# Kernel optimization log

Hardware: AMD Instinct MI355X
Metric: run time of the kernel (lower is better)

## Reference

```python
import jax, jax.numpy as jnp
import numpy as np

B, T, D, E, K = 4, 2048, 1024, 8, 2

def setup_inputs() -> dict:
    key = jax.random.key(0)
    ks = jax.random.split(key, 4)
    scale = 1.0 / np.sqrt(D)
    return {
        "input_feat": jax.random.normal(ks[0], (B, T, D), dtype=jnp.float32),
        "delta": jax.random.normal(ks[1], (B, T, D), dtype=jnp.float32),
        "gate_W": jax.random.normal(ks[2], (E, D), dtype=jnp.float32) * scale,
        "gate_b": jnp.zeros((E,), dtype=jnp.float32),
        "expert_W": jax.random.normal(ks[3], (E, D, D), dtype=jnp.float32) * scale,
        "expert_b": jnp.zeros((E, D), dtype=jnp.float32),
    }

def reference(input_feat, delta, gate_W, gate_b, expert_W, expert_b):
    # Gating: logits [B,T,E], top-k over experts, softmax over the k logits
    gate_logits = jnp.einsum("btd,ed->bte", input_feat, gate_W) + gate_b
    topk_vals, topk_idx = jax.lax.top_k(gate_logits, K)          # [B,T,K]
    topk_weights = jax.nn.softmax(topk_vals, axis=-1)            # [B,T,K]

    # Dense per-expert linear on delta: [B,T,D,E] (torch Linear: x @ W.T + b)
    expert_outputs = jnp.einsum("btd,efd->btfe", delta, expert_W) + expert_b.T

    # Gather top-k expert outputs and weighted-combine
    idx = jnp.broadcast_to(topk_idx[:, :, None, :], (B, T, D, K))
    topk_outputs = jnp.take_along_axis(expert_outputs, idx, axis=-1)  # [B,T,D,K]
    weighted_output = jnp.sum(topk_outputs * topk_weights[:, :, None, :], axis=-1)
    return weighted_output
```

## Files before the change

### kernel.cpp

```cpp
#include <hip/hip_runtime.h>
#include <stdint.h>

#define NTOK 8192
#define D 1024
#define E 8
#define BM 128
#define BN 128
#define BK 64

typedef __attribute__((ext_vector_type(8))) short short8;
typedef __attribute__((ext_vector_type(4))) float f32x4;

__device__ __forceinline__ ushort f2bf(float f) {
  uint32_t x = __float_as_uint(f);
  x += 0x7FFFu + ((x >> 16) & 1u);
  return (ushort)(x >> 16);
}

#define NW4 2097152
#define ND4 2097152
#define NO4 2097152
__global__ __launch_bounds__(256) void convert_zero_kernel(
    const float* __restrict__ expert_W, const float* __restrict__ delta,
    ushort* __restrict__ Wb, ushort* __restrict__ Db,
    float* __restrict__ out, int* __restrict__ cnt) {
  int i = blockIdx.x * 256 + threadIdx.x;
  if (i < E) cnt[i] = 0;
  if (i < NW4) {
    float4 v = ((const float4*)expert_W)[i];
    ushort4 u; u.x = f2bf(v.x); u.y = f2bf(v.y); u.z = f2bf(v.z); u.w = f2bf(v.w);
    ((ushort4*)Wb)[i] = u;
  } else if (i < NW4 + ND4) {
    int j = i - NW4;
    float4 v = ((const float4*)delta)[j];
    ushort4 u; u.x = f2bf(v.x); u.y = f2bf(v.y); u.z = f2bf(v.z); u.w = f2bf(v.w);
    ((ushort4*)Db)[j] = u;
  } else {
    int j = i - NW4 - ND4;
    ((float4*)out)[j] = (float4){0.f, 0.f, 0.f, 0.f};
  }
}

__global__ __launch_bounds__(256) void gate_topk_kernel(
    const float* __restrict__ x, const float* __restrict__ gW,
    const float* __restrict__ gb,
    int* __restrict__ idx01, float2* __restrict__ w01) {
  int wave = threadIdx.x >> 6;
  int lane = threadIdx.x & 63;
  int t = blockIdx.x * 4 + wave;

  const float4* xr = (const float4*)(x + (size_t)t * D) + lane * 4;
  float acc[E];
#pragma unroll
  for (int e = 0; e < E; ++e) acc[e] = 0.f;
#pragma unroll
  for (int q = 0; q < 4; ++q) {
    float4 xv = xr[q];
#pragma unroll
    for (int e = 0; e < E; ++e) {
      float4 wv = ((const float4*)(gW + e * D))[lane * 4 + q];
      acc[e] += xv.x * wv.x + xv.y * wv.y + xv.z * wv.z + xv.w * wv.w;
    }
  }
#pragma unroll
  for (int e = 0; e < E; ++e) {
    float v = acc[e];
#pragma unroll
    for (int off = 32; off > 0; off >>= 1) v += __shfl_xor(v, off, 64);
    acc[e] = v;
  }
  if (lane == 0) {
    float lg[E];
#pragma unroll
    for (int e = 0; e < E; ++e) lg[e] = acc[e] + gb[e];
    int i0 = 0; float v0 = lg[0];
#pragma unroll
    for (int e = 1; e < E; ++e) { if (lg[e] > v0) { v0 = lg[e]; i0 = e; } }
    int i1 = -1; float v1 = -1e30f;
#pragma unroll
    for (int e = 0; e < E; ++e) { if (e != i0 && lg[e] > v1) { v1 = lg[e]; i1 = e; } }
    float e1 = __expf(v1 - v0);
    float inv = 1.f / (1.f + e1);
    idx01[t] = i0 | (i1 << 16);
    w01[t] = make_float2(inv, e1 * inv);
  }
}

__global__ __launch_bounds__(256) void bin_kernel(
    const int* __restrict__ idx01, const float2* __restrict__ w01,
    int* __restrict__ cnt, int* __restrict__ list, float* __restrict__ wlist) {
  __shared__ int hist[E];
  __shared__ int base[E];
  int tid = threadIdx.x;
  int t = blockIdx.x * 256 + tid;
  if (tid < E) hist[tid] = 0;
  __syncthreads();

  int packed = idx01[t];
  float2 w = w01[t];
  int i0 = packed & 0xFFFF, i1 = packed >> 16;
  int r0 = atomicAdd(&hist[i0], 1);
  int r1 = atomicAdd(&hist[i1], 1);
  __syncthreads();
  if (tid < E) base[tid] = atomicAdd(&cnt[tid], hist[tid]);
  __syncthreads();

  int s0 = base[i0] + r0;
  list[i0 * NTOK + s0] = t; wlist[i0 * NTOK + s0] = w.x;
  int s1 = base[i1] + r1;
  list[i1 * NTOK + s1] = t; wlist[i1 * NTOK + s1] = w.y;
}

__global__ __launch_bounds__(256) void moe_gemm_kernel(
    const ushort* __restrict__ Db, const ushort* __restrict__ Wb,
    const float* __restrict__ eb, const int* __restrict__ cnt,
    const int* __restrict__ list, const float* __restrict__ wlist,
    float* __restrict__ out) {
  int bx = blockIdx.x;
  int mt = bx >> 6;
  int rem = bx & 63;
  int e = rem >> 3;
  int nt = rem & 7;
  int M = cnt[e];
  int m0 = mt * BM;
  if (m0 >= M) return;
  int n0 = nt * BN;

  __shared__ ushort As[BM * BK];
  __shared__ ushort Bs[BN * BK];

  int tid = threadIdx.x;
  int wave = tid >> 6;
  int lane = tid & 63;
  int wm = wave >> 1;
  int wn = wave & 1;
  const int c = lane & 15;
  const int q = lane >> 4;

  const int* listE = list + e * NTOK;

  int rloc = lane >> 3;
  int gglob = (lane & 7) ^ rloc;
  const ushort* aptr[4];
  ushort* alds[4];
#pragma unroll
  for (int p = 0; p < 4; ++p) {
    int r = m0 + wave * 32 + p * 8 + rloc;
    int tok = listE[r < M ? r : m0];
    aptr[p] = Db + (size_t)tok * D + gglob * 8;
    alds[p] = &As[(wave * 32 + p * 8) * BK];
  }
  const ushort* WbE = Wb + ((size_t)e << 20);
  const ushort* bptr[4];
  ushort* blds[4];
#pragma unroll
  for (int p = 0; p < 4; ++p) {
    int row = n0 + wave * 32 + p * 8 + rloc;
    bptr[p] = WbE + (size_t)row * D + gglob * 8;
    blds[p] = &Bs[(wave * 32 + p * 8) * BK];
  }

  f32x4 acc[4][4];
#pragma unroll
  for (int i = 0; i < 4; ++i)
#pragma unroll
    for (int j = 0; j < 4; ++j)
      acc[i][j] = (f32x4){0.f, 0.f, 0.f, 0.f};

  for (int k0 = 0; k0 < D; k0 += BK) {
#pragma unroll
    for (int p = 0; p < 4; ++p)
      __builtin_amdgcn_global_load_lds(
          (const __attribute__((address_space(1))) void*)(aptr[p] + k0),
          (__attribute__((address_space(3))) void*)alds[p], 16, 0, 0);
#pragma unroll
    for (int p = 0; p < 4; ++p)
      __builtin_amdgcn_global_load_lds(
          (const __attribute__((address_space(1))) void*)(bptr[p] + k0),
          (__attribute__((address_space(3))) void*)blds[p], 16, 0, 0);
    __syncthreads();

#pragma unroll
    for (int s = 0; s < 2; ++s) {
      int sw = (((s * 4 + q) ^ (c & 7)) * 8);
      short8 a[4], b[4];
#pragma unroll
      for (int i = 0; i < 4; ++i)
        a[i] = *(const short8*)&As[(wm * 64 + i * 16 + c) * BK + sw];
#pragma unroll
      for (int j = 0; j < 4; ++j)
        b[j] = *(const short8*)&Bs[(wn * 64 + j * 16 + c) * BK + sw];
#pragma unroll
      for (int i = 0; i < 4; ++i)
#pragma unroll
        for (int j = 0; j < 4; ++j)
          acc[i][j] = __builtin_amdgcn_mfma_f32_16x16x32_bf16(a[i], b[j], acc[i][j], 0, 0, 0);
    }
    __syncthreads();
  }

  float bias[4];
#pragma unroll
  for (int j = 0; j < 4; ++j)
    bias[j] = eb[e * D + n0 + wn * 64 + j * 16 + c];
  const float* wlE = wlist + e * NTOK;
#pragma unroll
  for (int i = 0; i < 4; ++i) {
#pragma unroll
    for (int r = 0; r < 4; ++r) {
      int m = m0 + wm * 64 + i * 16 + q * 4 + r;
      if (m < M) {
        int tok = listE[m];
        float w = wlE[m];
        float* orow = out + (size_t)tok * D + n0 + wn * 64 + c;
#pragma unroll
        for (int j = 0; j < 4; ++j)
          atomicAdd(&orow[j * 16], (acc[i][j][r] + bias[j]) * w);
      }
    }
  }
}

extern "C" void kernel_launch(void* const* d_in, const int* in_sizes, int n_in,
                              void* d_out, int out_size, void* d_ws, size_t ws_size,
                              hipStream_t stream) {
  const float* input_feat = (const float*)d_in[0];
  const float* delta      = (const float*)d_in[1];
  const float* gate_W     = (const float*)d_in[2];
  const float* gate_b     = (const float*)d_in[3];
  const float* expert_W   = (const float*)d_in[4];
  const float* expert_b   = (const float*)d_in[5];
  float* out = (float*)d_out;

  char* ws = (char*)d_ws;
  ushort* Wb    = (ushort*)ws;
  ushort* Db    = (ushort*)(ws + 16777216);
  char*   meta  = ws + 2 * 16777216;
  int*    cnt   = (int*)meta;
  int*    list  = (int*)(meta + 256);
  float*  wlist = (float*)(meta + 256 + NTOK * E * 4);
  int*    idx01 = (int*)(meta + 256 + 2 * NTOK * E * 4);
  float2* w01   = (float2*)(meta + 256 + 2 * NTOK * E * 4 + NTOK * 4);

  int total4 = NW4 + ND4 + NO4;
  convert_zero_kernel<<<total4 / 256, 256, 0, stream>>>(expert_W, delta, Wb, Db, out, cnt);
  gate_topk_kernel<<<NTOK / 4, 256, 0, stream>>>(input_feat, gate_W, gate_b, idx01, w01);
  bin_kernel<<<NTOK / 256, 256, 0, stream>>>(idx01, w01, cnt, list, wlist);
  moe_gemm_kernel<<<(NTOK / BM) * 64, 256, 0, stream>>>(
      Db, Wb, expert_b, cnt, list, wlist, out);
}
```

Before: 263.0 us.

## Enlarge MoE GEMM tiles to 256x256 and double-buffer LDS k-tiles

```diff
diff --git a/kernel.cpp b/kernel.cpp
--- a/kernel.cpp
+++ b/kernel.cpp
@@ -4,9 +4,11 @@
 #define NTOK 8192
 #define D 1024
 #define E 8
-#define BM 128
-#define BN 128
+#define BM 256
+#define BN 256
 #define BK 64
+#define NKT (D / BK)
+#define BUFE (BM * BK)
 
 typedef __attribute__((ext_vector_type(8))) short short8;
 typedef __attribute__((ext_vector_type(4))) float f32x4;
@@ -111,29 +113,29 @@
   list[i1 * NTOK + s1] = t; wlist[i1 * NTOK + s1] = w.y;
 }
 
-__global__ __launch_bounds__(256) void moe_gemm_kernel(
+__global__ __launch_bounds__(512) void moe_gemm_kernel(
     const ushort* __restrict__ Db, const ushort* __restrict__ Wb,
     const float* __restrict__ eb, const int* __restrict__ cnt,
     const int* __restrict__ list, const float* __restrict__ wlist,
     float* __restrict__ out) {
   int bx = blockIdx.x;
-  int mt = bx >> 6;
-  int rem = bx & 63;
-  int e = rem >> 3;
-  int nt = rem & 7;
+  int mt = bx >> 5;
+  int rem = bx & 31;
+  int e = rem >> 2;
+  int nt = rem & 3;
   int M = cnt[e];
   int m0 = mt * BM;
   if (m0 >= M) return;
   int n0 = nt * BN;
 
-  __shared__ ushort As[BM * BK];
-  __shared__ ushort Bs[BN * BK];
+  __shared__ ushort As[2 * BM * BK];
+  __shared__ ushort Bs[2 * BN * BK];
 
   int tid = threadIdx.x;
   int wave = tid >> 6;
   int lane = tid & 63;
-  int wm = wave >> 1;
-  int wn = wave & 1;
+  int wm = wave >> 2;
+  int wn = wave & 3;
   const int c = lane & 15;
   const int q = lane >> 4;
 
@@ -160,38 +162,53 @@
     blds[p] = &Bs[(wave * 32 + p * 8) * BK];
   }
 
-  f32x4 acc[4][4];
-#pragma unroll
-  for (int i = 0; i < 4; ++i)
+  f32x4 acc[8][4];
+#pragma unroll
+  for (int i = 0; i < 8; ++i)
 #pragma unroll
     for (int j = 0; j < 4; ++j)
       acc[i][j] = (f32x4){0.f, 0.f, 0.f, 0.f};
 
-  for (int k0 = 0; k0 < D; k0 += BK) {
-#pragma unroll
-    for (int p = 0; p < 4; ++p)
-      __builtin_amdgcn_global_load_lds(
-          (const __attribute__((address_space(1))) void*)(aptr[p] + k0),
-          (__attribute__((address_space(3))) void*)alds[p], 16, 0, 0);
-#pragma unroll
-    for (int p = 0; p < 4; ++p)
-      __builtin_amdgcn_global_load_lds(
-          (const __attribute__((address_space(1))) void*)(bptr[p] + k0),
-          (__attribute__((address_space(3))) void*)blds[p], 16, 0, 0);
-    __syncthreads();
-
+#pragma unroll
+  for (int p = 0; p < 4; ++p) {
+    __builtin_amdgcn_global_load_lds(
+        (const __attribute__((address_space(1))) void*)(aptr[p]),
+        (__attribute__((address_space(3))) void*)(alds[p]), 16, 0, 0);
+    __builtin_amdgcn_global_load_lds(
+        (const __attribute__((address_space(1))) void*)(bptr[p]),
+        (__attribute__((address_space(3))) void*)(blds[p]), 16, 0, 0);
+  }
+  __syncthreads();
+
+  for (int kt = 0; kt < NKT; ++kt) {
+    int cur = (kt & 1) * BUFE;
+    if (kt < NKT - 1) {
+      int nxt = ((kt + 1) & 1) * BUFE;
+      int kk = (kt + 1) * BK;
+#pragma unroll
+      for (int p = 0; p < 4; ++p) {
+        __builtin_amdgcn_global_load_lds(
+            (const __attribute__((address_space(1))) void*)(aptr[p] + kk),
+            (__attribute__((address_space(3))) void*)(alds[p] + nxt), 16, 0, 0);
+        __builtin_amdgcn_global_load_lds(
+            (const __attribute__((address_space(1))) void*)(bptr[p] + kk),
+            (__attribute__((address_space(3))) void*)(blds[p] + nxt), 16, 0, 0);
+      }
+    }
+    const ushort* Ab = As + cur;
+    const ushort* Bb = Bs + cur;
 #pragma unroll
     for (int s = 0; s < 2; ++s) {
       int sw = (((s * 4 + q) ^ (c & 7)) * 8);
-      short8 a[4], b[4];
-#pragma unroll
-      for (int i = 0; i < 4; ++i)
-        a[i] = *(const short8*)&As[(wm * 64 + i * 16 + c) * BK + sw];
+      short8 a[8], b[4];
+#pragma unroll
+      for (int i = 0; i < 8; ++i)
+        a[i] = *(const short8*)&Ab[(wm * 128 + i * 16 + c) * BK + sw];
 #pragma unroll
       for (int j = 0; j < 4; ++j)
-        b[j] = *(const short8*)&Bs[(wn * 64 + j * 16 + c) * BK + sw];
-#pragma unroll
-      for (int i = 0; i < 4; ++i)
+        b[j] = *(const short8*)&Bb[(wn * 64 + j * 16 + c) * BK + sw];
+#pragma unroll
+      for (int i = 0; i < 8; ++i)
 #pragma unroll
         for (int j = 0; j < 4; ++j)
           acc[i][j] = __builtin_amdgcn_mfma_f32_16x16x32_bf16(a[i], b[j], acc[i][j], 0, 0, 0);
@@ -205,10 +222,10 @@
     bias[j] = eb[e * D + n0 + wn * 64 + j * 16 + c];
   const float* wlE = wlist + e * NTOK;
 #pragma unroll
-  for (int i = 0; i < 4; ++i) {
+  for (int i = 0; i < 8; ++i) {
 #pragma unroll
     for (int r = 0; r < 4; ++r) {
-      int m = m0 + wm * 64 + i * 16 + q * 4 + r;
+      int m = m0 + wm * 128 + i * 16 + q * 4 + r;
       if (m < M) {
         int tok = listE[m];
         float w = wlE[m];
@@ -246,6 +263,6 @@
   convert_zero_kernel<<<total4 / 256, 256, 0, stream>>>(expert_W, delta, Wb, Db, out, cnt);
   gate_topk_kernel<<<NTOK / 4, 256, 0, stream>>>(input_feat, gate_W, gate_b, idx01, w01);
   bin_kernel<<<NTOK / 256, 256, 0, stream>>>(idx01, w01, cnt, list, wlist);
-  moe_gemm_kernel<<<(NTOK / BM) * 64, 256, 0, stream>>>(
+  moe_gemm_kernel<<<(NTOK / BM) * E * (D / BN), 512, 0, stream>>>(
       Db, Wb, expert_b, cnt, list, wlist, out);
 }
```

Measured after the change: 281.0 us. 6.8% more time.
